# Kernel tuning notes

Hardware: AMD Instinct MI355X
Metric: run time of the kernel (lower is better)

## Reference

```python
import jax, jax.numpy as jnp
import numpy as np

_SAMPLING_EPS = 1e-5


def setup_inputs() -> dict:
    key = jax.random.key(0)
    k1, k2, k3, k4, k5, k6 = jax.random.split(key, 6)
    B, V = 128, 128000
    return {
        "logits": jax.random.normal(k1, (B, V), dtype=jnp.float32),
        "temperature": jax.random.uniform(k2, (B,), dtype=jnp.float32),
        "min_p": jax.random.uniform(k3, (B,), dtype=jnp.float32),
        "top_k": jax.random.randint(k4, (B,), 0, 1024),
        "top_p": jax.random.uniform(k5, (B,), dtype=jnp.float32),
        "q": jax.random.uniform(k6, (B, V), dtype=jnp.float32),
        "num_logprobs": 20,
    }


def reference(logits, temperature, min_p, top_k, top_p, q, num_logprobs):
    B, V = logits.shape
    # raw logprobs computed BEFORE any processing (as in Sampler.forward)
    raw_logprobs = jax.nn.log_softmax(logits, axis=-1)
    # greedy sample on unscaled logits
    greedy = jnp.argmax(logits, axis=-1)
    # temperature scaling
    lt = logits / temperature[:, None]
    # min-p filtering
    probs = jax.nn.softmax(lt, axis=-1)
    max_p = jnp.max(probs, axis=-1, keepdims=True)
    lt = jnp.where(probs >= min_p[:, None] * max_p, lt, -jnp.inf)
    # top-k / top-p filtering on ascending-sorted logits (vLLM style)
    idx = jnp.argsort(lt, axis=-1)                       # ascending
    ls = jnp.take_along_axis(lt, idx, axis=-1)
    k = jnp.clip(top_k, 1, V)
    kth = jnp.take_along_axis(ls, (V - k)[:, None], axis=-1)  # k-th largest value
    ls = jnp.where(ls < kth, -jnp.inf, ls)
    ps = jax.nn.softmax(ls, axis=-1)
    csum = jnp.cumsum(ps, axis=-1)
    pmask = csum <= (1.0 - top_p)[:, None]
    pmask = pmask.at[:, -1].set(False)                   # always keep the max token
    ls = jnp.where(pmask, -jnp.inf, ls)
    inv = jnp.argsort(idx, axis=-1)                      # inverse permutation (scatter back)
    filtered = jnp.take_along_axis(ls, inv, axis=-1)
    # exponential-race sampling: argmax(probs / Exp(1)) ~ Categorical(probs)
    probs2 = jax.nn.softmax(filtered, axis=-1)
    expo = -jnp.log(jnp.clip(q, 1e-10, 1.0))
    rand_sampled = jnp.argmax(probs2 / expo, axis=-1)
    sampled = jnp.where(temperature < _SAMPLING_EPS, greedy, rand_sampled)
    # gather_logprobs: top-k logprobs + sampled-token logprob + rank
    topk_lp, topk_idx = jax.lax.top_k(raw_logprobs, num_logprobs)
    tok_lp = jnp.take_along_axis(raw_logprobs, sampled[:, None], axis=-1)  # (B,1)
    ranks = jnp.sum(raw_logprobs >= tok_lp, axis=-1)
    out_idx = jnp.concatenate([sampled[:, None], topk_idx], axis=1).astype(jnp.int32)
    out_lp = jnp.concatenate([tok_lp, topk_lp], axis=1)  # (B, num_logprobs+1)
    return (sampled[:, None].astype(jnp.int32), out_idx, out_lp, ranks)
```

## Files before the change

### kernel.cpp

```cpp
#include <hip/hip_runtime.h>
#include <math.h>

#define NB 1024
#define C_CAP 2048
#define BLK1 512
#define BLK2 512
#define NW2 (BLK2 / 64)
#define NWAVES1 (BLK1 / 64)
#define WSEG 512
#define LCAP2 2048
#define FLOORB 682
#define BIN_SCALE ((float)NB / 12.0f)
#define BOUND 1.9921875f

__device__ __forceinline__ int bin_of(float x) {
  int b = (int)floorf((x + 6.0f) * BIN_SCALE);
  return min(max(b, 0), NB - 1);
}
__device__ __forceinline__ unsigned long long pack_vi(float v, int idx) {
  return ((unsigned long long)__float_as_uint(v) << 32) | (unsigned int)idx;
}
__device__ __forceinline__ unsigned long long okey(float v, int idx) {
  unsigned int u = __float_as_uint(v);
  u = (u & 0x80000000u) ? ~u : (u | 0x80000000u);
  return ((unsigned long long)u << 32) | (unsigned long long)(0x7fffffffu - (unsigned int)idx);
}
__device__ __forceinline__ float okey_val(unsigned long long k) {
  unsigned int hi = (unsigned int)(k >> 32);
  unsigned int u = (hi & 0x80000000u) ? (hi & 0x7fffffffu) : ~hi;
  return __uint_as_float(u);
}
__device__ __forceinline__ int okey_idx(unsigned long long k) {
  return (int)(0x7fffffffu - (unsigned int)k);
}

__global__ __launch_bounds__(BLK1)
void k1_scan(const float* __restrict__ logits, int V, int halfElems,
             unsigned long long* __restrict__ plist, int* __restrict__ pcnt,
             float* __restrict__ psum) {
  const int row = blockIdx.y, half = blockIdx.x, tid = threadIdx.x;
  const int wave = tid >> 6, lane = tid & 63;
  const float* lrow = logits + (size_t)row * V;
  const int start = half * halfElems;
  const int end = min(start + halfElems, V);
  __shared__ unsigned long long seg[NWAVES1][WSEG];
  __shared__ int wcnt[NWAVES1];
  __shared__ int wbase[NWAVES1];
  __shared__ float s_sum;
  if (tid < NWAVES1) wcnt[tid] = 0;
  if (tid == 0) s_sum = 0.0f;
  __syncthreads();

  float s0 = 0.0f, s1 = 0.0f, s2 = 0.0f, s3 = 0.0f;
  const int n = max(end - start, 0);
  const int n4 = n >> 2;
  const float4* p4 = (const float4*)(lrow + start);
  int i = tid;
  for (; i + 3 * BLK1 < n4; i += 4 * BLK1) {
    float4 a0 = p4[i], a1 = p4[i + BLK1], a2 = p4[i + 2 * BLK1], a3 = p4[i + 3 * BLK1];
    float va[16] = {a0.x, a0.y, a0.z, a0.w, a1.x, a1.y, a1.z, a1.w,
                    a2.x, a2.y, a2.z, a2.w, a3.x, a3.y, a3.z, a3.w};
    #pragma unroll
    for (int c2 = 0; c2 < 16; c2++) {
      float x = va[c2];
      float e = __expf(fminf(x, 70.0f) - 6.0f);
      if (c2 < 4) s0 += e; else if (c2 < 8) s1 += e; else if (c2 < 12) s2 += e; else s3 += e;
      if (x >= BOUND) {
        int p = atomicAdd(&wcnt[wave], 1);
        if (p < WSEG) seg[wave][p] = pack_vi(x, start + ((i + (c2 >> 2) * BLK1) << 2) + (c2 & 3));
      }
    }
  }
  for (; i < n4; i += BLK1) {
    float4 a = p4[i];
    float va[4] = {a.x, a.y, a.z, a.w};
    #pragma unroll
    for (int c2 = 0; c2 < 4; c2++) {
      float x = va[c2];
      s0 += __expf(fminf(x, 70.0f) - 6.0f);
      if (x >= BOUND) {
        int p = atomicAdd(&wcnt[wave], 1);
        if (p < WSEG) seg[wave][p] = pack_vi(x, start + (i << 2) + c2);
      }
    }
  }
  for (int j = (n4 << 2) + tid; j < n; j += BLK1) {
    float x = lrow[start + j];
    s0 += __expf(fminf(x, 70.0f) - 6.0f);
    if (x >= BOUND) {
      int p = atomicAdd(&wcnt[wave], 1);
      if (p < WSEG) seg[wave][p] = pack_vi(x, start + j);
    }
  }
  float s = (s0 + s1) + (s2 + s3);
  for (int o = 32; o > 0; o >>= 1) s += __shfl_down(s, o, 64);
  if (lane == 0) atomicAdd(&s_sum, s);
  __syncthreads();

  if (tid == 0) {
    int b = 0, ov = 0;
    for (int w = 0; w < NWAVES1; w++) {
      wbase[w] = b;
      int cw = wcnt[w];
      if (cw > WSEG) { ov = 1; cw = WSEG; }
      b += cw;
    }
    const size_t rc = (size_t)row * 2 + half;
    psum[rc] = s_sum;
    pcnt[rc] = (ov || b > LCAP2) ? (LCAP2 + 1) : b;
  }
  __syncthreads();
  {
    int cw = min(wcnt[wave], WSEG);
    int base = wbase[wave];
    unsigned long long* prow = plist + ((size_t)row * 2 + half) * LCAP2;
    for (int j = lane; j < cw; j += 64) {
      int pos = base + j;
      if (pos < LCAP2) prow[pos] = seg[wave][j];
    }
  }
}

__global__ __launch_bounds__(BLK2)
void k2_fused(const float* __restrict__ logits,
              const float* __restrict__ temperature,
              const float* __restrict__ min_p,
              const int* __restrict__ top_k,
              const float* __restrict__ top_p,
              const float* __restrict__ q,
              const int* __restrict__ nl_ptr,
              int V, int B,
              const unsigned long long* __restrict__ plist,
              const int* __restrict__ pcnt,
              const float* __restrict__ psum,
              float* __restrict__ out) {
  const int row = blockIdx.x, tid = threadIdx.x;
  const int wave = tid >> 6, lane = tid & 63;
  __shared__ int h[NB + 1];
  __shared__ int cur[NB];
  __shared__ unsigned long long lst[2 * LCAP2];
  __shared__ unsigned long long bkt[C_CAP];
  __shared__ float sv[C_CAP];
  __shared__ int   si[C_CAP];
  __shared__ float ss[C_CAP];
  __shared__ float wtot[NW2];
  __shared__ float wb_sc[NW2], wb_vl[NW2];
  __shared__ int   wb_id[NW2];
  __shared__ int   s_n1, s_n2, s_rank, s_b;
  __shared__ float s_lse;

  for (int i = tid; i < NB; i += BLK2) { h[i] = 0; cur[i] = 0; }
  if (tid == 0) {
    h[NB] = 0; s_b = 0;
    s_n1 = 0x7fffffff; s_n2 = 0x7fffffff; s_rank = 0x7fffffff;
    s_lse = 6.0f + logf(psum[(size_t)row * 2] + psum[(size_t)row * 2 + 1]);
  }
  __syncthreads();

  const int p0 = pcnt[(size_t)row * 2], p1 = pcnt[(size_t)row * 2 + 1];
  const int c0 = min(p0, LCAP2), c1 = min(p1, LCAP2);
  const int tot = c0 + c1;
  int nl = nl_ptr[0];
  int ke = top_k[row]; ke = min(max(ke, 1), V);
  const int Kp = max(ke, nl);
  const bool fast = (p0 <= LCAP2) && (p1 <= LCAP2) && (tot >= Kp);

  const float* lrow = logits + (size_t)row * V;
  const int n4 = V >> 2;
  const float4* p4 = (const float4*)lrow;

  if (fast) {
    const unsigned long long* pr0 = plist + (size_t)row * 2 * LCAP2;
    const unsigned long long* pr1 = pr0 + LCAP2;
    for (int j = tid; j < c0; j += BLK2) lst[j] = pr0[j];
    for (int j = tid; j < c1; j += BLK2) lst[c0 + j] = pr1[j];
    __syncthreads();
    for (int j = tid; j < tot; j += BLK2) {
      float x = __uint_as_float((unsigned int)(lst[j] >> 32));
      atomicAdd(&h[bin_of(x)], 1);
    }
  } else {
    for (int ii = tid; ii < n4; ii += BLK2) {
      float4 a4 = p4[ii];
      atomicAdd(&h[bin_of(a4.x)], 1); atomicAdd(&h[bin_of(a4.y)], 1);
      atomicAdd(&h[bin_of(a4.z)], 1); atomicAdd(&h[bin_of(a4.w)], 1);
    }
    for (int j = (n4 << 2) + tid; j < V; j += BLK2)
      atomicAdd(&h[bin_of(lrow[j])], 1);
  }
  __syncthreads();

  if (wave == 0) {
    int hl[16];
    const int b16 = lane << 4;
    int lsum = 0;
    #pragma unroll
    for (int k = 0; k < 16; k++) { hl[k] = h[b16 + k]; lsum += hl[k]; }
    int s = lsum;
    #pragma unroll
    for (int o = 1; o < 64; o <<= 1) {
      int t = __shfl_down(s, o, 64);
      if (lane + o < 64) s += t;
    }
    int run = s - lsum;
    int bst = 0;
    #pragma unroll
    for (int k = 15; k >= 0; k--) {
      run += hl[k];
      h[b16 + k] = run;
      if (run >= Kp) bst = max(bst, b16 + k);
    }
    #pragma unroll
    for (int o = 1; o < 64; o <<= 1) {
      int t = __shfl_down(bst, o, 64);
      if (lane + o < 64) bst = max(bst, t);
    }
    if (lane == 0) s_b = bst;
  }
  __syncthreads();
  const int bstar = s_b;
  int c = min(h[bstar], C_CAP); if (c < 1) c = 1;

  if (fast) {
    for (int j = tid; j < tot; j += BLK2) {
      unsigned long long kk = lst[j];
      float x = __uint_as_float((unsigned int)(kk >> 32));
      int idx = (int)(unsigned int)kk;
      int b = bin_of(x);
      if (b >= bstar) {
        int a = atomicAdd(&cur[b], 1);
        int pos = h[b + 1] + a;
        if (pos < C_CAP) bkt[pos] = okey(x, idx);
      }
    }
  } else {
    for (int ii = tid; ii < n4; ii += BLK2) {
      float4 a4 = p4[ii];
      float va[4] = {a4.x, a4.y, a4.z, a4.w};
      #pragma unroll
      for (int c2 = 0; c2 < 4; c2++) {
        int b = bin_of(va[c2]);
        if (b >= bstar) {
          int a = atomicAdd(&cur[b], 1);
          int pos = h[b + 1] + a;
          if (pos < C_CAP) bkt[pos] = okey(va[c2], (ii << 2) + c2);
        }
      }
    }
    for (int j = (n4 << 2) + tid; j < V; j += BLK2) {
      float x = lrow[j];
      int b = bin_of(x);
      if (b >= bstar) {
        int a = atomicAdd(&cur[b], 1);
        int pos = h[b + 1] + a;
        if (pos < C_CAP) bkt[pos] = okey(x, j);
      }
    }
  }
  __syncthreads();

  for (int pos = tid; pos < c; pos += BLK2) {
    unsigned long long k0 = bkt[pos];
    float v = okey_val(k0);
    int b = bin_of(v);
    int gs = h[b + 1];
    int ge = min(h[b], c);
    int rk = 0;
    for (int j = gs; j < ge; j++) if (bkt[j] > k0) rk++;
    int fin = gs + rk;
    sv[fin] = v; si[fin] = okey_idx(k0);
  }
  __syncthreads();

  float temp = temperature[row];
  bool ug = (temp < 1e-5f);
  float rt = 1.0f / (ug ? 1.0f : temp);
  float mp = min_p[row], tp = top_p[row];
  ke = min(ke, c);
  float v0 = sv[0];
  float lt0 = v0 * rt;

  float ltk = sv[ke - 1] * rt;
  float kth = (expf(ltk - lt0) >= mp) ? ltk : -INFINITY;

  {
    int lm = 0x7fffffff;
    for (int ii = tid; ii < c; ii += BLK2) {
      float ltj = sv[ii] * rt;
      if (!((expf(ltj - lt0) >= mp) && (ltj >= kth))) { lm = ii; break; }
    }
    #pragma unroll
    for (int o = 1; o < 64; o <<= 1) {
      int t = __shfl_down(lm, o, 64);
      if (lane + o < 64) lm = min(lm, t);
    }
    if (lane == 0 && lm != 0x7fffffff) atomicMin(&s_n1, lm);
  }
  __syncthreads();
  int n1 = min(s_n1, c); if (n1 < 1) n1 = 1;

  int L = (c + BLK2 - 1) / BLK2;
  int base = tid * L;
  int lim = min(base + L, c);
  float run = 0.0f;
  for (int j = base; j < lim; j++) {
    float pj = (j < n1) ? expf(sv[j] * rt - lt0) : 0.0f;
    run += pj; ss[j] = run;
  }
  float v = run;
  #pragma unroll
  for (int o = 1; o < 64; o <<= 1) {
    float t = __shfl_up(v, o, 64);
    if (lane >= o) v += t;
  }
  if (lane == 63) wtot[wave] = v;
  __syncthreads();
  float woff = 0.0f;
  for (int w2 = 0; w2 < wave; w2++) woff += wtot[w2];
  float myoff = woff + (v - run);
  for (int j = base; j < lim; j++) ss[j] += myoff;
  __syncthreads();
  float Z1 = ss[n1 - 1];

  {
    int lm = 0x7fffffff;
    for (int ii = tid; ii < n1; ii += BLK2) {
      if (ii > 0 && !((1.0f - ss[ii - 1] / Z1) > (1.0f - tp))) { lm = ii; break; }
    }
    #pragma unroll
    for (int o = 1; o < 64; o <<= 1) {
      int t = __shfl_down(lm, o, 64);
      if (lane + o < 64) lm = min(lm, t);
    }
    if (lane == 0 && lm != 0x7fffffff) atomicMin(&s_n2, lm);
  }
  __syncthreads();
  int n2 = min(s_n2, n1); if (n2 < 1) n2 = 1;
  float Z2 = ss[n2 - 1];

  const float* qrow = q + (size_t)row * V;
  float bsc = -INFINITY; int bidx = 0x7fffffff; float bval = 0.0f;
  for (int ii = tid; ii < n2; ii += BLK2) {
    float pj = expf(sv[ii] * rt - lt0);
    float qv = qrow[si[ii]];
    qv = fminf(fmaxf(qv, 1e-10f), 1.0f);
    float sc = (pj / Z2) / (-logf(qv));
    if (sc > bsc || (sc == bsc && si[ii] < bidx)) { bsc = sc; bidx = si[ii]; bval = sv[ii]; }
  }
  #pragma unroll
  for (int o = 1; o < 64; o <<= 1) {
    float sc2 = __shfl_down(bsc, o, 64);
    int   id2 = __shfl_down(bidx, o, 64);
    float vl2 = __shfl_down(bval, o, 64);
    if (lane + o < 64) {
      if (sc2 > bsc || (sc2 == bsc && id2 < bidx)) { bsc = sc2; bidx = id2; bval = vl2; }
    }
  }
  if (lane == 0) { wb_sc[wave] = bsc; wb_id[wave] = bidx; wb_vl[wave] = bval; }
  __syncthreads();
  float fsc = wb_sc[0]; int fid = wb_id[0]; float fvl = wb_vl[0];
  #pragma unroll
  for (int w2 = 1; w2 < NW2; w2++) {
    float sc2 = wb_sc[w2]; int id2 = wb_id[w2]; float vl2 = wb_vl[w2];
    if (sc2 > fsc || (sc2 == fsc && id2 < fid)) { fsc = sc2; fid = id2; fvl = vl2; }
  }
  int sampled = ug ? si[0] : fid;
  float val_s = ug ? sv[0] : fvl;
  float lse = s_lse;
  float tok_lp = val_s - lse;

  {
    int lm = 0x7fffffff;
    for (int ii = tid; ii < c; ii += BLK2)
      if (!((sv[ii] - lse) >= tok_lp)) { lm = ii; break; }
    #pragma unroll
    for (int o = 1; o < 64; o <<= 1) {
      int t = __shfl_down(lm, o, 64);
      if (lane + o < 64) lm = min(lm, t);
    }
    if (lane == 0 && lm != 0x7fffffff) atomicMin(&s_rank, lm);
  }
  __syncthreads();
  int rank = min(s_rank, c);

  int W = nl + 1;
  if (tid == 0) {
    out[row] = (float)sampled;
    out[B + row * W] = (float)sampled;
    out[B + B * W + row * W] = tok_lp;
    out[B + 2 * B * W + row] = (float)rank;
  }
  for (int t = tid; t < nl; t += BLK2) {
    out[B + row * W + 1 + t] = (float)si[t];
    out[B + B * W + row * W + 1 + t] = sv[t] - lse;
  }
}

extern "C" void kernel_launch(void* const* d_in, const int* in_sizes, int n_in,
                              void* d_out, int out_size, void* d_ws, size_t ws_size,
                              hipStream_t stream) {
  const float* logits      = (const float*)d_in[0];
  const float* temperature = (const float*)d_in[1];
  const float* min_p       = (const float*)d_in[2];
  const int*   top_k       = (const int*)d_in[3];
  const float* top_p       = (const float*)d_in[4];
  const float* q           = (const float*)d_in[5];
  const int*   nl_ptr      = (const int*)d_in[6];

  int B = in_sizes[1];
  int V = in_sizes[0] / B;
  float* out = (float*)d_out;
  int halfElems = (((V + 1) / 2) + 3) & ~3;

  unsigned char* w = (unsigned char*)d_ws;
  unsigned long long* plist = (unsigned long long*)w; w += (size_t)B * 2 * LCAP2 * sizeof(unsigned long long);
  int* pcnt = (int*)w;                                w += (size_t)B * 2 * sizeof(int);
  float* psum = (float*)w;                            w += (size_t)B * 2 * sizeof(float);

  hipLaunchKernelGGL(k1_scan, dim3(2, B), dim3(BLK1), 0, stream,
                     logits, V, halfElems, plist, pcnt, psum);
  hipLaunchKernelGGL(k2_fused, dim3(B), dim3(BLK2), 0, stream,
                     logits, temperature, min_p, top_k, top_p, q, nl_ptr,
                     V, B, plist, pcnt, psum, out);
}
```

Measured before the change: 157.2 us.

## Fuse scan and select kernels into one cooperative launch with grid sync

Moves both phases into a single cooperative kernel. The shared-memory layouts of the two phases are unioned, and phase 1 is separated from phase 2 by a grid-wide barrier, which removes the second kernel launch and its inter-kernel gap. The cooperative launch needs all 256 blocks to be resident at once, and the union shared struct is large. If the cooperative launch fails, the code falls back to the old two-kernel path. The grid barrier and the heavier per-block shared memory could cost more than the launch gap they remove.

```diff
diff --git a/kernel.cpp b/kernel.cpp
--- a/kernel.cpp
+++ b/kernel.cpp
@@ -1,4 +1,5 @@
 #include <hip/hip_runtime.h>
+#include <hip/hip_cooperative_groups.h>
 #include <math.h>
 
 #define NB 1024
@@ -9,7 +10,6 @@
 #define NWAVES1 (BLK1 / 64)
 #define WSEG 512
 #define LCAP2 2048
-#define FLOORB 682
 #define BIN_SCALE ((float)NB / 12.0f)
 #define BOUND 1.9921875f
 
@@ -34,21 +34,39 @@
   return (int)(0x7fffffffu - (unsigned int)k);
 }
 
-__global__ __launch_bounds__(BLK1)
-void k1_scan(const float* __restrict__ logits, int V, int halfElems,
-             unsigned long long* __restrict__ plist, int* __restrict__ pcnt,
-             float* __restrict__ psum) {
-  const int row = blockIdx.y, half = blockIdx.x, tid = threadIdx.x;
+struct P1Shared {
+  unsigned long long seg[NWAVES1][WSEG];
+  int wcnt[NWAVES1];
+  int wbase[NWAVES1];
+  float s_sum;
+};
+struct P2Shared {
+  unsigned long long lst[2 * LCAP2];
+  unsigned long long bkt[C_CAP];
+  float sv[C_CAP];
+  int   si[C_CAP];
+  float ss[C_CAP];
+  int h[NB + 1];
+  int cur[NB];
+  float wtot[NW2];
+  float wb_sc[NW2], wb_vl[NW2];
+  int   wb_id[NW2];
+  int   s_n1, s_n2, s_rank, s_b;
+  float s_lse;
+};
+union CoopShared { P1Shared p1; P2Shared p2; };
+
+__device__ void phase1_body(const float* __restrict__ logits, int V, int halfElems,
+                            unsigned long long* __restrict__ plist,
+                            int* __restrict__ pcnt, float* __restrict__ psum,
+                            int row, int half, P1Shared* S) {
+  const int tid = threadIdx.x;
   const int wave = tid >> 6, lane = tid & 63;
   const float* lrow = logits + (size_t)row * V;
   const int start = half * halfElems;
   const int end = min(start + halfElems, V);
-  __shared__ unsigned long long seg[NWAVES1][WSEG];
-  __shared__ int wcnt[NWAVES1];
-  __shared__ int wbase[NWAVES1];
-  __shared__ float s_sum;
-  if (tid < NWAVES1) wcnt[tid] = 0;
-  if (tid == 0) s_sum = 0.0f;
+  if (tid < NWAVES1) S->wcnt[tid] = 0;
+  if (tid == 0) S->s_sum = 0.0f;
   __syncthreads();
 
   float s0 = 0.0f, s1 = 0.0f, s2 = 0.0f, s3 = 0.0f;
@@ -66,8 +84,8 @@
       float e = __expf(fminf(x, 70.0f) - 6.0f);
       if (c2 < 4) s0 += e; else if (c2 < 8) s1 += e; else if (c2 < 12) s2 += e; else s3 += e;
       if (x >= BOUND) {
-        int p = atomicAdd(&wcnt[wave], 1);
-        if (p < WSEG) seg[wave][p] = pack_vi(x, start + ((i + (c2 >> 2) * BLK1) << 2) + (c2 & 3));
+        int p = atomicAdd(&S->wcnt[wave], 1);
+        if (p < WSEG) S->seg[wave][p] = pack_vi(x, start + ((i + (c2 >> 2) * BLK1) << 2) + (c2 & 3));
       }
     }
   }
@@ -79,8 +97,8 @@
       float x = va[c2];
       s0 += __expf(fminf(x, 70.0f) - 6.0f);
       if (x >= BOUND) {
-        int p = atomicAdd(&wcnt[wave], 1);
-        if (p < WSEG) seg[wave][p] = pack_vi(x, start + (i << 2) + c2);
+        int p = atomicAdd(&S->wcnt[wave], 1);
+        if (p < WSEG) S->seg[wave][p] = pack_vi(x, start + (i << 2) + c2);
       }
     }
   }
@@ -88,37 +106,338 @@
     float x = lrow[start + j];
     s0 += __expf(fminf(x, 70.0f) - 6.0f);
     if (x >= BOUND) {
-      int p = atomicAdd(&wcnt[wave], 1);
-      if (p < WSEG) seg[wave][p] = pack_vi(x, start + j);
+      int p = atomicAdd(&S->wcnt[wave], 1);
+      if (p < WSEG) S->seg[wave][p] = pack_vi(x, start + j);
     }
   }
   float s = (s0 + s1) + (s2 + s3);
   for (int o = 32; o > 0; o >>= 1) s += __shfl_down(s, o, 64);
-  if (lane == 0) atomicAdd(&s_sum, s);
+  if (lane == 0) atomicAdd(&S->s_sum, s);
   __syncthreads();
 
   if (tid == 0) {
     int b = 0, ov = 0;
     for (int w = 0; w < NWAVES1; w++) {
-      wbase[w] = b;
-      int cw = wcnt[w];
+      S->wbase[w] = b;
+      int cw = S->wcnt[w];
       if (cw > WSEG) { ov = 1; cw = WSEG; }
       b += cw;
     }
     const size_t rc = (size_t)row * 2 + half;
-    psum[rc] = s_sum;
+    psum[rc] = S->s_sum;
     pcnt[rc] = (ov || b > LCAP2) ? (LCAP2 + 1) : b;
   }
   __syncthreads();
   {
-    int cw = min(wcnt[wave], WSEG);
-    int base = wbase[wave];
+    int cw = min(S->wcnt[wave], WSEG);
+    int base = S->wbase[wave];
     unsigned long long* prow = plist + ((size_t)row * 2 + half) * LCAP2;
     for (int j = lane; j < cw; j += 64) {
       int pos = base + j;
-      if (pos < LCAP2) prow[pos] = seg[wave][j];
-    }
-  }
+      if (pos < LCAP2) prow[pos] = S->seg[wave][j];
+    }
+  }
+}
+
+__device__ void phase2_body(const float* __restrict__ logits,
+                            const float* __restrict__ temperature,
+                            const float* __restrict__ min_p,
+                            const int* __restrict__ top_k,
+                            const float* __restrict__ top_p,
+                            const float* __restrict__ q,
+                            const int* __restrict__ nl_ptr,
+                            int V, int B,
+                            const unsigned long long* __restrict__ plist,
+                            const int* __restrict__ pcnt,
+                            const float* __restrict__ psum,
+                            float* __restrict__ out,
+                            int row, P2Shared* S) {
+  const int tid = threadIdx.x;
+  const int wave = tid >> 6, lane = tid & 63;
+  int* h = S->h;
+  int* cur = S->cur;
+  unsigned long long* lst = S->lst;
+  unsigned long long* bkt = S->bkt;
+  float* sv = S->sv;
+  int*   si = S->si;
+  float* ss = S->ss;
+
+  for (int i = tid; i < NB; i += BLK2) { h[i] = 0; cur[i] = 0; }
+  if (tid == 0) {
+    h[NB] = 0; S->s_b = 0;
+    S->s_n1 = 0x7fffffff; S->s_n2 = 0x7fffffff; S->s_rank = 0x7fffffff;
+    S->s_lse = 6.0f + logf(psum[(size_t)row * 2] + psum[(size_t)row * 2 + 1]);
+  }
+  __syncthreads();
+
+  const int p0 = pcnt[(size_t)row * 2], p1 = pcnt[(size_t)row * 2 + 1];
+  const int c0 = min(p0, LCAP2), c1 = min(p1, LCAP2);
+  const int tot = c0 + c1;
+  int nl = nl_ptr[0];
+  int ke = top_k[row]; ke = min(max(ke, 1), V);
+  const int Kp = max(ke, nl);
+  const bool fast = (p0 <= LCAP2) && (p1 <= LCAP2) && (tot >= Kp);
+
+  const float* lrow = logits + (size_t)row * V;
+  const int n4 = V >> 2;
+  const float4* p4 = (const float4*)lrow;
+
+  if (fast) {
+    const unsigned long long* pr0 = plist + (size_t)row * 2 * LCAP2;
+    const unsigned long long* pr1 = pr0 + LCAP2;
+    for (int j = tid; j < c0; j += BLK2) lst[j] = pr0[j];
+    for (int j = tid; j < c1; j += BLK2) lst[c0 + j] = pr1[j];
+    __syncthreads();
+    for (int j = tid; j < tot; j += BLK2) {
+      float x = __uint_as_float((unsigned int)(lst[j] >> 32));
+      atomicAdd(&h[bin_of(x)], 1);
+    }
+  } else {
+    for (int ii = tid; ii < n4; ii += BLK2) {
+      float4 a4 = p4[ii];
+      atomicAdd(&h[bin_of(a4.x)], 1); atomicAdd(&h[bin_of(a4.y)], 1);
+      atomicAdd(&h[bin_of(a4.z)], 1); atomicAdd(&h[bin_of(a4.w)], 1);
+    }
+    for (int j = (n4 << 2) + tid; j < V; j += BLK2)
+      atomicAdd(&h[bin_of(lrow[j])], 1);
+  }
+  __syncthreads();
+
+  if (wave == 0) {
+    int hl[16];
+    const int b16 = lane << 4;
+    int lsum = 0;
+    #pragma unroll
+    for (int k = 0; k < 16; k++) { hl[k] = h[b16 + k]; lsum += hl[k]; }
+    int s = lsum;
+    #pragma unroll
+    for (int o = 1; o < 64; o <<= 1) {
+      int t = __shfl_down(s, o, 64);
+      if (lane + o < 64) s += t;
+    }
+    int run = s - lsum;
+    int bst = 0;
+    #pragma unroll
+    for (int k = 15; k >= 0; k--) {
+      run += hl[k];
+      h[b16 + k] = run;
+      if (run >= Kp) bst = max(bst, b16 + k);
+    }
+    #pragma unroll
+    for (int o = 1; o < 64; o <<= 1) {
+      int t = __shfl_down(bst, o, 64);
+      if (lane + o < 64) bst = max(bst, t);
+    }
+    if (lane == 0) S->s_b = bst;
+  }
+  __syncthreads();
+  const int bstar = S->s_b;
+  int c = min(h[bstar], C_CAP); if (c < 1) c = 1;
+
+  if (fast) {
+    for (int j = tid; j < tot; j += BLK2) {
+      unsigned long long kk = lst[j];
+      float x = __uint_as_float((unsigned int)(kk >> 32));
+      int idx = (int)(unsigned int)kk;
+      int b = bin_of(x);
+      if (b >= bstar) {
+        int a = atomicAdd(&cur[b], 1);
+        int pos = h[b + 1] + a;
+        if (pos < C_CAP) bkt[pos] = okey(x, idx);
+      }
+    }
+  } else {
+    for (int ii = tid; ii < n4; ii += BLK2) {
+      float4 a4 = p4[ii];
+      float va[4] = {a4.x, a4.y, a4.z, a4.w};
+      #pragma unroll
+      for (int c2 = 0; c2 < 4; c2++) {
+        int b = bin_of(va[c2]);
+        if (b >= bstar) {
+          int a = atomicAdd(&cur[b], 1);
+          int pos = h[b + 1] + a;
+          if (pos < C_CAP) bkt[pos] = okey(va[c2], (ii << 2) + c2);
+        }
+      }
+    }
+    for (int j = (n4 << 2) + tid; j < V; j += BLK2) {
+      float x = lrow[j];
+      int b = bin_of(x);
+      if (b >= bstar) {
+        int a = atomicAdd(&cur[b], 1);
+        int pos = h[b + 1] + a;
+        if (pos < C_CAP) bkt[pos] = okey(x, j);
+      }
+    }
+  }
+  __syncthreads();
+
+  for (int pos = tid; pos < c; pos += BLK2) {
+    unsigned long long k0 = bkt[pos];
+    float v = okey_val(k0);
+    int b = bin_of(v);
+    int gs = h[b + 1];
+    int ge = min(h[b], c);
+    int rk = 0;
+    for (int j = gs; j < ge; j++) if (bkt[j] > k0) rk++;
+    int fin = gs + rk;
+    sv[fin] = v; si[fin] = okey_idx(k0);
+  }
+  __syncthreads();
+
+  float temp = temperature[row];
+  bool ug = (temp < 1e-5f);
+  float rt = 1.0f / (ug ? 1.0f : temp);
+  float mp = min_p[row], tp = top_p[row];
+  ke = min(ke, c);
+  float v0 = sv[0];
+  float lt0 = v0 * rt;
+
+  float ltk = sv[ke - 1] * rt;
+  float kth = (expf(ltk - lt0) >= mp) ? ltk : -INFINITY;
+
+  {
+    int lm = 0x7fffffff;
+    for (int ii = tid; ii < c; ii += BLK2) {
+      float ltj = sv[ii] * rt;
+      if (!((expf(ltj - lt0) >= mp) && (ltj >= kth))) { lm = ii; break; }
+    }
+    #pragma unroll
+    for (int o = 1; o < 64; o <<= 1) {
+      int t = __shfl_down(lm, o, 64);
+      if (lane + o < 64) lm = min(lm, t);
+    }
+    if (lane == 0 && lm != 0x7fffffff) atomicMin(&S->s_n1, lm);
+  }
+  __syncthreads();
+  int n1 = min(S->s_n1, c); if (n1 < 1) n1 = 1;
+
+  int L = (c + BLK2 - 1) / BLK2;
+  int base = tid * L;
+  int lim = min(base + L, c);
+  float run = 0.0f;
+  for (int j = base; j < lim; j++) {
+    float pj = (j < n1) ? expf(sv[j] * rt - lt0) : 0.0f;
+    run += pj; ss[j] = run;
+  }
+  float v = run;
+  #pragma unroll
+  for (int o = 1; o < 64; o <<= 1) {
+    float t = __shfl_up(v, o, 64);
+    if (lane >= o) v += t;
+  }
+  if (lane == 63) S->wtot[wave] = v;
+  __syncthreads();
+  float woff = 0.0f;
+  for (int w2 = 0; w2 < wave; w2++) woff += S->wtot[w2];
+  float myoff = woff + (v - run);
+  for (int j = base; j < lim; j++) ss[j] += myoff;
+  __syncthreads();
+  float Z1 = ss[n1 - 1];
+
+  {
+    int lm = 0x7fffffff;
+    for (int ii = tid; ii < n1; ii += BLK2) {
+      if (ii > 0 && !((1.0f - ss[ii - 1] / Z1) > (1.0f - tp))) { lm = ii; break; }
+    }
+    #pragma unroll
+    for (int o = 1; o < 64; o <<= 1) {
+      int t = __shfl_down(lm, o, 64);
+      if (lane + o < 64) lm = min(lm, t);
+    }
+    if (lane == 0 && lm != 0x7fffffff) atomicMin(&S->s_n2, lm);
+  }
+  __syncthreads();
+  int n2 = min(S->s_n2, n1); if (n2 < 1) n2 = 1;
+  float Z2 = ss[n2 - 1];
+
+  const float* qrow = q + (size_t)row * V;
+  float bsc = -INFINITY; int bidx = 0x7fffffff; float bval = 0.0f;
+  for (int ii = tid; ii < n2; ii += BLK2) {
+    float pj = expf(sv[ii] * rt - lt0);
+    float qv = qrow[si[ii]];
+    qv = fminf(fmaxf(qv, 1e-10f), 1.0f);
+    float sc = (pj / Z2) / (-logf(qv));
+    if (sc > bsc || (sc == bsc && si[ii] < bidx)) { bsc = sc; bidx = si[ii]; bval = sv[ii]; }
+  }
+  #pragma unroll
+  for (int o = 1; o < 64; o <<= 1) {
+    float sc2 = __shfl_down(bsc, o, 64);
+    int   id2 = __shfl_down(bidx, o, 64);
+    float vl2 = __shfl_down(bval, o, 64);
+    if (lane + o < 64) {
+      if (sc2 > bsc || (sc2 == bsc && id2 < bidx)) { bsc = sc2; bidx = id2; bval = vl2; }
+    }
+  }
+  if (lane == 0) { S->wb_sc[wave] = bsc; S->wb_id[wave] = bidx; S->wb_vl[wave] = bval; }
+  __syncthreads();
+  float fsc = S->wb_sc[0]; int fid = S->wb_id[0]; float fvl = S->wb_vl[0];
+  #pragma unroll
+  for (int w2 = 1; w2 < NW2; w2++) {
+    float sc2 = S->wb_sc[w2]; int id2 = S->wb_id[w2]; float vl2 = S->wb_vl[w2];
+    if (sc2 > fsc || (sc2 == fsc && id2 < fid)) { fsc = sc2; fid = id2; fvl = vl2; }
+  }
+  int sampled = ug ? si[0] : fid;
+  float val_s = ug ? sv[0] : fvl;
+  float lse = S->s_lse;
+  float tok_lp = val_s - lse;
+
+  {
+    int lm = 0x7fffffff;
+    for (int ii = tid; ii < c; ii += BLK2)
+      if (!((sv[ii] - lse) >= tok_lp)) { lm = ii; break; }
+    #pragma unroll
+    for (int o = 1; o < 64; o <<= 1) {
+      int t = __shfl_down(lm, o, 64);
+      if (lane + o < 64) lm = min(lm, t);
+    }
+    if (lane == 0 && lm != 0x7fffffff) atomicMin(&S->s_rank, lm);
+  }
+  __syncthreads();
+  int rank = min(S->s_rank, c);
+
+  int W = nl + 1;
+  if (tid == 0) {
+    out[row] = (float)sampled;
+    out[B + row * W] = (float)sampled;
+    out[B + B * W + row * W] = tok_lp;
+    out[B + 2 * B * W + row] = (float)rank;
+  }
+  for (int t = tid; t < nl; t += BLK2) {
+    out[B + row * W + 1 + t] = (float)si[t];
+    out[B + B * W + row * W + 1 + t] = sv[t] - lse;
+  }
+}
+
+__global__ __launch_bounds__(BLK1)
+void sampler_coop(const float* __restrict__ logits,
+                  const float* __restrict__ temperature,
+                  const float* __restrict__ min_p,
+                  const int* __restrict__ top_k,
+                  const float* __restrict__ top_p,
+                  const float* __restrict__ q,
+                  const int* __restrict__ nl_ptr,
+                  int V, int B, int halfElems,
+                  unsigned long long* __restrict__ plist,
+                  int* __restrict__ pcnt,
+                  float* __restrict__ psum,
+                  float* __restrict__ out) {
+  __shared__ CoopShared S;
+  const int row1 = blockIdx.x >> 1, half = blockIdx.x & 1;
+  phase1_body(logits, V, halfElems, plist, pcnt, psum, row1, half, &S.p1);
+  __threadfence();
+  cooperative_groups::this_grid().sync();
+  if ((int)blockIdx.x < B)
+    phase2_body(logits, temperature, min_p, top_k, top_p, q, nl_ptr,
+                V, B, plist, pcnt, psum, out, blockIdx.x, &S.p2);
+}
+
+__global__ __launch_bounds__(BLK1)
+void k1_scan(const float* __restrict__ logits, int V, int halfElems,
+             unsigned long long* __restrict__ plist, int* __restrict__ pcnt,
+             float* __restrict__ psum) {
+  __shared__ P1Shared S;
+  phase1_body(logits, V, halfElems, plist, pcnt, psum, blockIdx.y, blockIdx.x, &S);
 }
 
 __global__ __launch_bounds__(BLK2)
@@ -134,266 +453,9 @@
               const int* __restrict__ pcnt,
               const float* __restrict__ psum,
               float* __restrict__ out) {
-  const int row = blockIdx.x, tid = threadIdx.x;
-  const int wave = tid >> 6, lane = tid & 63;
-  __shared__ int h[NB + 1];
-  __shared__ int cur[NB];
-  __shared__ unsigned long long lst[2 * LCAP2];
-  __shared__ unsigned long long bkt[C_CAP];
-  __shared__ float sv[C_CAP];
-  __shared__ int   si[C_CAP];
-  __shared__ float ss[C_CAP];
-  __shared__ float wtot[NW2];
-  __shared__ float wb_sc[NW2], wb_vl[NW2];
-  __shared__ int   wb_id[NW2];
-  __shared__ int   s_n1, s_n2, s_rank, s_b;
-  __shared__ float s_lse;
-
-  for (int i = tid; i < NB; i += BLK2) { h[i] = 0; cur[i] = 0; }
-  if (tid == 0) {
-    h[NB] = 0; s_b = 0;
-    s_n1 = 0x7fffffff; s_n2 = 0x7fffffff; s_rank = 0x7fffffff;
-    s_lse = 6.0f + logf(psum[(size_t)row * 2] + psum[(size_t)row * 2 + 1]);
-  }
-  __syncthreads();
-
-  const int p0 = pcnt[(size_t)row * 2], p1 = pcnt[(size_t)row * 2 + 1];
-  const int c0 = min(p0, LCAP2), c1 = min(p1, LCAP2);
-  const int tot = c0 + c1;
-  int nl = nl_ptr[0];
-  int ke = top_k[row]; ke = min(max(ke, 1), V);
-  const int Kp = max(ke, nl);
-  const bool fast = (p0 <= LCAP2) && (p1 <= LCAP2) && (tot >= Kp);
-
-  const float* lrow = logits + (size_t)row * V;
-  const int n4 = V >> 2;
-  const float4* p4 = (const float4*)lrow;
-
-  if (fast) {
-    const unsigned long long* pr0 = plist + (size_t)row * 2 * LCAP2;
-    const unsigned long long* pr1 = pr0 + LCAP2;
-    for (int j = tid; j < c0; j += BLK2) lst[j] = pr0[j];
-    for (int j = tid; j < c1; j += BLK2) lst[c0 + j] = pr1[j];
-    __syncthreads();
-    for (int j = tid; j < tot; j += BLK2) {
-      float x = __uint_as_float((unsigned int)(lst[j] >> 32));
-      atomicAdd(&h[bin_of(x)], 1);
-    }
-  } else {
-    for (int ii = tid; ii < n4; ii += BLK2) {
-      float4 a4 = p4[ii];
-      atomicAdd(&h[bin_of(a4.x)], 1); atomicAdd(&h[bin_of(a4.y)], 1);
-      atomicAdd(&h[bin_of(a4.z)], 1); atomicAdd(&h[bin_of(a4.w)], 1);
-    }
-    for (int j = (n4 << 2) + tid; j < V; j += BLK2)
-      atomicAdd(&h[bin_of(lrow[j])], 1);
-  }
-  __syncthreads();
-
-  if (wave == 0) {
-    int hl[16];
-    const int b16 = lane << 4;
-    int lsum = 0;
-    #pragma unroll
-    for (int k = 0; k < 16; k++) { hl[k] = h[b16 + k]; lsum += hl[k]; }
-    int s = lsum;
-    #pragma unroll
-    for (int o = 1; o < 64; o <<= 1) {
-      int t = __shfl_down(s, o, 64);
-      if (lane + o < 64) s += t;
-    }
-    int run = s - lsum;
-    int bst = 0;
-    #pragma unroll
-    for (int k = 15; k >= 0; k--) {
-      run += hl[k];
-      h[b16 + k] = run;
-      if (run >= Kp) bst = max(bst, b16 + k);
-    }
-    #pragma unroll
-    for (int o = 1; o < 64; o <<= 1) {
-      int t = __shfl_down(bst, o, 64);
-      if (lane + o < 64) bst = max(bst, t);
-    }
-    if (lane == 0) s_b = bst;
-  }
-  __syncthreads();
-  const int bstar = s_b;
-  int c = min(h[bstar], C_CAP); if (c < 1) c = 1;
-
-  if (fast) {
-    for (int j = tid; j < tot; j += BLK2) {
-      unsigned long long kk = lst[j];
-      float x = __uint_as_float((unsigned int)(kk >> 32));
-      int idx = (int)(unsigned int)kk;
-      int b = bin_of(x);
-      if (b >= bstar) {
-        int a = atomicAdd(&cur[b], 1);
-        int pos = h[b + 1] + a;
-        if (pos < C_CAP) bkt[pos] = okey(x, idx);
-      }
-    }
-  } else {
-    for (int ii = tid; ii < n4; ii += BLK2) {
-      float4 a4 = p4[ii];
-      float va[4] = {a4.x, a4.y, a4.z, a4.w};
-      #pragma unroll
-      for (int c2 = 0; c2 < 4; c2++) {
-        int b = bin_of(va[c2]);
-        if (b >= bstar) {
-          int a = atomicAdd(&cur[b], 1);
-          int pos = h[b + 1] + a;
-          if (pos < C_CAP) bkt[pos] = okey(va[c2], (ii << 2) + c2);
-        }
-      }
-    }
-    for (int j = (n4 << 2) + tid; j < V; j += BLK2) {
-      float x = lrow[j];
-      int b = bin_of(x);
-      if (b >= bstar) {
-        int a = atomicAdd(&cur[b], 1);
-        int pos = h[b + 1] + a;
-        if (pos < C_CAP) bkt[pos] = okey(x, j);
-      }
-    }
-  }
-  __syncthreads();
-
-  for (int pos = tid; pos < c; pos += BLK2) {
-    unsigned long long k0 = bkt[pos];
-    float v = okey_val(k0);
-    int b = bin_of(v);
-    int gs = h[b + 1];
-    int ge = min(h[b], c);
-    int rk = 0;
-    for (int j = gs; j < ge; j++) if (bkt[j] > k0) rk++;
-    int fin = gs + rk;
-    sv[fin] = v; si[fin] = okey_idx(k0);
-  }
-  __syncthreads();
-
-  float temp = temperature[row];
-  bool ug = (temp < 1e-5f);
-  float rt = 1.0f / (ug ? 1.0f : temp);
-  float mp = min_p[row], tp = top_p[row];
-  ke = min(ke, c);
-  float v0 = sv[0];
-  float lt0 = v0 * rt;
-
-  float ltk = sv[ke - 1] * rt;
-  float kth = (expf(ltk - lt0) >= mp) ? ltk : -INFINITY;
-
-  {
-    int lm = 0x7fffffff;
-    for (int ii = tid; ii < c; ii += BLK2) {
-      float ltj = sv[ii] * rt;
-      if (!((expf(ltj - lt0) >= mp) && (ltj >= kth))) { lm = ii; break; }
-    }
-    #pragma unroll
-    for (int o = 1; o < 64; o <<= 1) {
-      int t = __shfl_down(lm, o, 64);
-      if (lane + o < 64) lm = min(lm, t);
-    }
-    if (lane == 0 && lm != 0x7fffffff) atomicMin(&s_n1, lm);
-  }
-  __syncthreads();
-  int n1 = min(s_n1, c); if (n1 < 1) n1 = 1;
-
-  int L = (c + BLK2 - 1) / BLK2;
-  int base = tid * L;
-  int lim = min(base + L, c);
-  float run = 0.0f;
-  for (int j = base; j < lim; j++) {
-    float pj = (j < n1) ? expf(sv[j] * rt - lt0) : 0.0f;
-    run += pj; ss[j] = run;
-  }
-  float v = run;
-  #pragma unroll
-  for (int o = 1; o < 64; o <<= 1) {
-    float t = __shfl_up(v, o, 64);
-    if (lane >= o) v += t;
-  }
-  if (lane == 63) wtot[wave] = v;
-  __syncthreads();
-  float woff = 0.0f;
-  for (int w2 = 0; w2 < wave; w2++) woff += wtot[w2];
-  float myoff = woff + (v - run);
-  for (int j = base; j < lim; j++) ss[j] += myoff;
-  __syncthreads();
-  float Z1 = ss[n1 - 1];
-
-  {
-    int lm = 0x7fffffff;
-    for (int ii = tid; ii < n1; ii += BLK2) {
-      if (ii > 0 && !((1.0f - ss[ii - 1] / Z1) > (1.0f - tp))) { lm = ii; break; }
-    }
-    #pragma unroll
-    for (int o = 1; o < 64; o <<= 1) {
-      int t = __shfl_down(lm, o, 64);
-      if (lane + o < 64) lm = min(lm, t);
-    }
-    if (lane == 0 && lm != 0x7fffffff) atomicMin(&s_n2, lm);
-  }
-  __syncthreads();
-  int n2 = min(s_n2, n1); if (n2 < 1) n2 = 1;
-  float Z2 = ss[n2 - 1];
-
-  const float* qrow = q + (size_t)row * V;
-  float bsc = -INFINITY; int bidx = 0x7fffffff; float bval = 0.0f;
-  for (int ii = tid; ii < n2; ii += BLK2) {
-    float pj = expf(sv[ii] * rt - lt0);
-    float qv = qrow[si[ii]];
-    qv = fminf(fmaxf(qv, 1e-10f), 1.0f);
-    float sc = (pj / Z2) / (-logf(qv));
-    if (sc > bsc || (sc == bsc && si[ii] < bidx)) { bsc = sc; bidx = si[ii]; bval = sv[ii]; }
-  }
-  #pragma unroll
-  for (int o = 1; o < 64; o <<= 1) {
-    float sc2 = __shfl_down(bsc, o, 64);
-    int   id2 = __shfl_down(bidx, o, 64);
-    float vl2 = __shfl_down(bval, o, 64);
-    if (lane + o < 64) {
-      if (sc2 > bsc || (sc2 == bsc && id2 < bidx)) { bsc = sc2; bidx = id2; bval = vl2; }
-    }
-  }
-  if (lane == 0) { wb_sc[wave] = bsc; wb_id[wave] = bidx; wb_vl[wave] = bval; }
-  __syncthreads();
-  float fsc = wb_sc[0]; int fid = wb_id[0]; float fvl = wb_vl[0];
-  #pragma unroll
-  for (int w2 = 1; w2 < NW2; w2++) {
-    float sc2 = wb_sc[w2]; int id2 = wb_id[w2]; float vl2 = wb_vl[w2];
-    if (sc2 > fsc || (sc2 == fsc && id2 < fid)) { fsc = sc2; fid = id2; fvl = vl2; }
-  }
-  int sampled = ug ? si[0] : fid;
-  float val_s = ug ? sv[0] : fvl;
-  float lse = s_lse;
-  float tok_lp = val_s - lse;
-
-  {
-    int lm = 0x7fffffff;
-    for (int ii = tid; ii < c; ii += BLK2)
-      if (!((sv[ii] - lse) >= tok_lp)) { lm = ii; break; }
-    #pragma unroll
-    for (int o = 1; o < 64; o <<= 1) {
-      int t = __shfl_down(lm, o, 64);
-      if (lane + o < 64) lm = min(lm, t);
-    }
-    if (lane == 0 && lm != 0x7fffffff) atomicMin(&s_rank, lm);
-  }
-  __syncthreads();
-  int rank = min(s_rank, c);
-
-  int W = nl + 1;
-  if (tid == 0) {
-    out[row] = (float)sampled;
-    out[B + row * W] = (float)sampled;
-    out[B + B * W + row * W] = tok_lp;
-    out[B + 2 * B * W + row] = (float)rank;
-  }
-  for (int t = tid; t < nl; t += BLK2) {
-    out[B + row * W + 1 + t] = (float)si[t];
-    out[B + B * W + row * W + 1 + t] = sv[t] - lse;
-  }
+  __shared__ P2Shared S;
+  phase2_body(logits, temperature, min_p, top_k, top_p, q, nl_ptr,
+              V, B, plist, pcnt, psum, out, blockIdx.x, &S);
 }
 
 extern "C" void kernel_launch(void* const* d_in, const int* in_sizes, int n_in,
@@ -417,9 +479,20 @@
   int* pcnt = (int*)w;                                w += (size_t)B * 2 * sizeof(int);
   float* psum = (float*)w;                            w += (size_t)B * 2 * sizeof(float);
 
-  hipLaunchKernelGGL(k1_scan, dim3(2, B), dim3(BLK1), 0, stream,
-                     logits, V, halfElems, plist, pcnt, psum);
-  hipLaunchKernelGGL(k2_fused, dim3(B), dim3(BLK2), 0, stream,
-                     logits, temperature, min_p, top_k, top_p, q, nl_ptr,
-                     V, B, plist, pcnt, psum, out);
-}
+  void* args[] = {
+    (void*)&logits, (void*)&temperature, (void*)&min_p, (void*)&top_k,
+    (void*)&top_p, (void*)&q, (void*)&nl_ptr, (void*)&V, (void*)&B,
+    (void*)&halfElems, (void*)&plist, (void*)&pcnt, (void*)&psum, (void*)&out
+  };
+  hipError_t err = hipLaunchCooperativeKernel((void*)sampler_coop,
+                                              dim3(2 * B), dim3(BLK1),
+                                              args, 0, stream);
+  if (err != hipSuccess) {
+    (void)hipGetLastError();
+    hipLaunchKernelGGL(k1_scan, dim3(2, B), dim3(BLK1), 0, stream,
+                       logits, V, halfElems, plist, pcnt, psum);
+    hipLaunchKernelGGL(k2_fused, dim3(B), dim3(BLK2), 0, stream,
+                       logits, temperature, min_p, top_k, top_p, q, nl_ptr,
+                       V, B, plist, pcnt, psum, out);
+  }
+}
```

Result: slower. 254.3 us (+61.8%).
